# Performance work log

Hardware: AMD Instinct MI355X
Metric: run time of the kernel (lower is better)

## Reference

```python
import jax, jax.numpy as jnp
import numpy as np

NQ = 8  # qubits per circuit (= d_k = n_qubits_ffn)
# Fixed realization of tq.RandomLayer(n_ops=8): 6 parametric rotations + 2 CNOTs
OPS = [("ry", 0), ("rx", 3), ("rz", 5), ("cx", (1, 4)), ("ry", 6), ("rx", 2), ("cx", (0, 7)), ("rz", 4)]
_CNOT = jnp.asarray(np.array([[1,0,0,0],[0,1,0,0],[0,0,0,1],[0,0,1,0]], dtype=np.complex64).reshape(2,2,2,2))
# signs[i, w] = +1 if bit of wire w in basis index i is 0, else -1 (PauliZ eigenvalue)
_idx = np.arange(2 ** NQ)
_bits = (_idx[:, None] >> (NQ - 1 - np.arange(NQ))) & 1
SIGNS = jnp.asarray((1 - 2 * _bits).astype(np.float32))

def _rot(kind, t):
    c = jnp.cos(t / 2).astype(jnp.complex64)
    s = jnp.sin(t / 2).astype(jnp.complex64)
    z = jnp.zeros_like(c)
    if kind == "rx":
        return jnp.stack([jnp.stack([c, -1j * s]), jnp.stack([-1j * s, c])])
    if kind == "ry":
        return jnp.stack([jnp.stack([c, -s]), jnp.stack([s, c])])
    tc = t.astype(jnp.complex64)
    return jnp.stack([jnp.stack([jnp.exp(-1j * tc / 2), z]), jnp.stack([z, jnp.exp(1j * tc / 2)])])

def _apply1(state, U, w):
    st = jnp.tensordot(U, state, axes=((1,), (w + 1,)))
    return jnp.moveaxis(st, 0, w + 1)

def _apply2(state, c, t):  # CNOT, requires c < t (true for OPS)
    st = jnp.tensordot(_CNOT, state, axes=((2, 3), (c + 1, t + 1)))
    return jnp.moveaxis(st, (0, 1), (c + 1, t + 1))

def qcircuit(angles, thetas):
    """angles: [N, NQ] data angles (RX encoding); thetas: [6] gate params.
    Returns PauliZ expectations [N, NQ] (float32)."""
    N = angles.shape[0]
    c = jnp.cos(angles / 2)
    s = jnp.sin(angles / 2)
    amp = jnp.stack([c.astype(jnp.complex64), (-1j) * s.astype(jnp.complex64)], axis=-1)  # [N, NQ, 2]
    # RX-encoded product state |psi> = prod_w RX(x_w)|0>
    state = amp[:, 0]
    for w in range(1, NQ):
        state = state[..., None] * amp[:, w].reshape((N,) + (1,) * w + (2,))
    pi = 0
    for kind, arg in OPS:
        if kind == "cx":
            state = _apply2(state, *arg)
        else:
            state = _apply1(state, _rot(kind, thetas[pi]), arg)
            pi += 1
    probs = jnp.abs(state.reshape(N, -1)) ** 2  # [N, 2^NQ]
    return probs @ SIGNS  # [N, NQ]

def _ln(x, g, b, eps=1e-5):
    m = x.mean(-1, keepdims=True)
    v = ((x - m) ** 2).mean(-1, keepdims=True)
    return (x - m) / jnp.sqrt(v + eps) * g + b

def setup_inputs() -> dict:
    key = jax.random.key(0)
    ks = jax.random.split(key, 8)
    B, S, E, FF = 4, 1024, 64, 256
    return {
        "x": jax.random.normal(ks[0], (B, S, E), dtype=jnp.float32),
        "attn_theta": jax.random.uniform(ks[1], (6,), dtype=jnp.float32, maxval=2 * np.pi),
        "Wc": jax.random.normal(ks[2], (E, E), dtype=jnp.float32) * 0.1,
        "bc": jnp.zeros((E,), jnp.float32),
        "g1": jnp.ones((E,), jnp.float32),
        "beta1": jnp.zeros((E,), jnp.float32),
        "ffn_theta": jax.random.uniform(ks[3], (6,), dtype=jnp.float32, maxval=2 * np.pi),
        "W1": jax.random.normal(ks[4], (NQ, FF), dtype=jnp.float32) * 0.3,
        "b1": jnp.zeros((FF,), jnp.float32),
        "W2": jax.random.normal(ks[5], (FF, E), dtype=jnp.float32) * 0.06,
        "b2": jnp.zeros((E,), jnp.float32),
        "g2": jnp.ones((E,), jnp.float32),
        "beta2": jnp.zeros((E,), jnp.float32),
    }

def reference(x, attn_theta, Wc, bc, g1, beta1, ffn_theta, W1, b1, W2, b2, g2, beta2):
    B, S, E = x.shape
    dk = NQ  # d_k = embed_dim // num_heads = 8
    # --- quantum multi-head attention (same qlayer shared across heads -> vectorize) ---
    q = qcircuit(x.reshape(B * S * (E // dk), dk), attn_theta)  # [B*S*H, dk]
    attn = q.reshape(B, S, E) @ Wc + bc
    y = _ln(x + attn, g1, beta1)
    # --- quantum FFN: encoder uses first NQ features of each token ---
    qf = qcircuit(y.reshape(B * S, E)[:, :NQ], ffn_theta)  # [B*S, NQ]
    h = jax.nn.relu(qf @ W1 + b1)
    ffn = (h @ W2 + b2).reshape(B, S, E)
    return _ln(y + ffn, g2, beta2)
```

## Files before the change

### kernel.cpp

```cpp
#include <hip/hip_runtime.h>


typedef _Float16 h2f   __attribute__((ext_vector_type(2)));
typedef _Float16 f16x8 __attribute__((ext_vector_type(8)));
typedef float    f32x4 __attribute__((ext_vector_type(4)));
typedef int      i32x4 __attribute__((ext_vector_type(4)));

__device__ __forceinline__ int pk(float a, float b) {
    return __builtin_bit_cast(int, __builtin_amdgcn_cvt_pkrtz(a, b));
}
__device__ __forceinline__ float fdot2i(int a, int b, float c) {
    return __builtin_amdgcn_fdot2(__builtin_bit_cast(h2f, a),
                                  __builtin_bit_cast(h2f, b), c, false);
}
__device__ __forceinline__ float rl_f(float v, int l) {
    return __int_as_float(__builtin_amdgcn_readlane(__float_as_int(v), l));
}
__device__ __forceinline__ f16x8 pack8(const float (&v)[8]) {
    i32x4 p;
    p.x = pk(v[0], v[1]);
    p.y = pk(v[2], v[3]);
    p.z = pk(v[4], v[5]);
    p.w = pk(v[6], v[7]);
    return __builtin_bit_cast(f16x8, p);
}
__device__ __forceinline__ void wave_sum2(float& a, float& b) {
#pragma unroll
    for (int m = 32; m > 0; m >>= 1) {
        a += __shfl_xor(a, m, 64);
        b += __shfl_xor(b, m, 64);
    }
}

__global__ __launch_bounds__(512, 2)
void qtb_fused11(const float* __restrict__ x,
                 const float* __restrict__ th_a,
                 const float* __restrict__ Wc,
                 const float* __restrict__ bc,
                 const float* __restrict__ g1,
                 const float* __restrict__ be1,
                 const float* __restrict__ th_f,
                 const float* __restrict__ W1,
                 const float* __restrict__ b1,
                 const float* __restrict__ W2,
                 const float* __restrict__ b2,
                 const float* __restrict__ g2,
                 const float* __restrict__ be2,
                 float* __restrict__ out)
{
    __shared__ __align__(16) int4      sW1[256];
    __shared__ __align__(16) _Float16  sZ[16][72];
    __shared__ __align__(16) float     sA[16][66];
    __shared__ __align__(16) _Float16  sH[16][264];
    __shared__ __align__(16) float     sO[16][66];

    const int tid  = threadIdx.x;
    const int lane = tid & 63;
    const int wv   = tid >> 6;
    const int w    = lane & 7;
    const int gb   = lane & ~7;
    const int tok0 = (blockIdx.x * 8 + wv) * 2;
    const int tl   = wv * 2;
    const int col  = lane & 15;
    const int kg   = lane >> 4;

    float xr[2];
#pragma unroll
    for (int t = 0; t < 2; ++t) xr[t] = x[(tok0 + t) * 64 + lane];

    float bfa[2][8];
    float bff[8][8];
    if (wv < 4) {
        const float* base = Wc + wv * 16 + col;
#pragma unroll
        for (int ks = 0; ks < 2; ++ks)
#pragma unroll
            for (int i = 0; i < 8; ++i)
                bfa[ks][i] = base[(ks * 32 + kg * 8 + i) * 64];
    } else {
        const float* base = W2 + (wv - 4) * 16 + col;
#pragma unroll
        for (int ks = 0; ks < 8; ++ks)
#pragma unroll
            for (int i = 0; i < 8; ++i)
                bff[ks][i] = base[(ks * 32 + kg * 8 + i) * 64];
    }

    if (tid < 64) {
        int j0 = tid * 4;
        float4 r[8];
#pragma unroll
        for (int k = 0; k < 8; ++k) r[k] = *(const float4*)&W1[k * 256 + j0];
        const float* f = (const float*)r;
#pragma unroll
        for (int j = 0; j < 4; ++j)
            sW1[j0 + j] = make_int4(pk(f[0 * 4 + j], f[4 * 4 + j]),
                                    pk(f[1 * 4 + j], f[5 * 4 + j]),
                                    pk(f[2 * 4 + j], f[6 * 4 + j]),
                                    pk(f[3 * 4 + j], f[7 * 4 + j]));
    }

    const float C0a = __cosf(th_a[0]);
    const float T1a = th_a[1];
    const float C3a = __cosf(th_a[3]);
    const float T4a = th_a[4];
    const float C0f = __cosf(th_f[0]);
    const float T1f = th_f[1];
    const float C3f = __cosf(th_f[3]);
    const float T4f = th_f[4];

    const float bcL = bc[lane], g1L = g1[lane], be1L = be1[lane];
    const float b2L = b2[lane], g2L = g2[lane], be2L = be2[lane];
    float b1L[4];
#pragma unroll
    for (int r = 0; r < 4; ++r) b1L[r] = b1[r * 64 + lane];

    const float dA = (w == 2) ? T4a : ((w == 3) ? T1a : 0.0f);
#pragma unroll
    for (int t = 0; t < 2; ++t) {
        float c  = __cosf(xr[t] + dA);
        float c0 = __shfl(c, gb, 64);
        float c1 = __shfl(c, gb + 1, 64);
        float zz = c * ((w == 0) ? C0a : ((w == 6) ? C3a : 1.0f));
        if (w == 4) zz = c * c1;
        if (w == 7) zz = C0a * c0 * c;
        sZ[tl + t][lane] = (_Float16)zz;
    }

    f16x8 bfrag[8];
    if (wv < 4) {
#pragma unroll
        for (int ks = 0; ks < 2; ++ks) bfrag[ks] = pack8(bfa[ks]);
    } else {
#pragma unroll
        for (int ks = 0; ks < 8; ++ks) bfrag[ks] = pack8(bff[ks]);
    }

    __syncthreads();

    if (wv < 4) {
        f32x4 cacc = {0.0f, 0.0f, 0.0f, 0.0f};
#pragma unroll
        for (int ks = 0; ks < 2; ++ks) {
            f16x8 af = *(const f16x8*)&sZ[col][ks * 32 + kg * 8];
            cacc = __builtin_amdgcn_mfma_f32_16x16x32_f16(af, bfrag[ks], cacc, 0, 0, 0);
        }
#pragma unroll
        for (int r = 0; r < 4; ++r)
            sA[kg * 4 + r][wv * 16 + col] = cacc[r];
    }

    __syncthreads();

    float y[2];
#pragma unroll
    for (int t = 0; t < 2; ++t) {
        float v = xr[t] + sA[tl + t][lane] + bcL;
        float s = v, s2 = v * v;
        wave_sum2(s, s2);
        float m   = s * 0.015625f;
        float var = s2 * 0.015625f - m * m;
        y[t] = (v - m) * rsqrtf(var + 1e-5f) * g1L + be1L;
    }

    int4 w1q[4];
#pragma unroll
    for (int r = 0; r < 4; ++r) w1q[r] = sW1[r * 64 + lane];

    const float dF = (w == 2) ? T4f : ((w == 3) ? T1f : 0.0f);
#pragma unroll
    for (int t = 0; t < 2; ++t) {
        float cy = __cosf(y[t] + dF);
        float c0 = rl_f(cy, 0);
        float c1 = rl_f(cy, 1);
        float qz = cy * ((w == 0) ? C0f : ((w == 6) ? C3f : 1.0f));
        if (w == 4) qz = cy * c1;
        if (w == 7) qz = C0f * c0 * cy;
        int qp0 = pk(rl_f(qz, 0), rl_f(qz, 4));
        int qp1 = pk(rl_f(qz, 1), rl_f(qz, 5));
        int qp2 = pk(rl_f(qz, 2), rl_f(qz, 6));
        int qp3 = pk(rl_f(qz, 3), rl_f(qz, 7));
#pragma unroll
        for (int r = 0; r < 4; ++r) {
            float a = b1L[r];
            a = fdot2i(qp0, w1q[r].x, a);
            a = fdot2i(qp1, w1q[r].y, a);
            a = fdot2i(qp2, w1q[r].z, a);
            a = fdot2i(qp3, w1q[r].w, a);
            sH[tl + t][r * 64 + lane] = (_Float16)fmaxf(a, 0.0f);
        }
    }

    __syncthreads();

    if (wv >= 4) {
        f32x4 cacc = {0.0f, 0.0f, 0.0f, 0.0f};
#pragma unroll
        for (int ks = 0; ks < 8; ++ks) {
            f16x8 af = *(const f16x8*)&sH[col][ks * 32 + kg * 8];
            cacc = __builtin_amdgcn_mfma_f32_16x16x32_f16(af, bfrag[ks], cacc, 0, 0, 0);
        }
#pragma unroll
        for (int r = 0; r < 4; ++r)
            sO[kg * 4 + r][(wv - 4) * 16 + col] = cacc[r];
    }

    __syncthreads();

#pragma unroll
    for (int t = 0; t < 2; ++t) {
        float v = y[t] + b2L + sO[tl + t][lane];
        float s = v, s2 = v * v;
        wave_sum2(s, s2);
        float m   = s * 0.015625f;
        float var = s2 * 0.015625f - m * m;
        out[(tok0 + t) * 64 + lane] = (v - m) * rsqrtf(var + 1e-5f) * g2L + be2L;
    }
}

extern "C" void kernel_launch(void* const* d_in, const int* in_sizes, int n_in,
                              void* d_out, int out_size, void* d_ws, size_t ws_size,
                              hipStream_t stream)
{
    const float* x   = (const float*)d_in[0];
    const float* at  = (const float*)d_in[1];
    const float* Wc  = (const float*)d_in[2];
    const float* bcp = (const float*)d_in[3];
    const float* g1  = (const float*)d_in[4];
    const float* be1 = (const float*)d_in[5];
    const float* ft  = (const float*)d_in[6];
    const float* W1  = (const float*)d_in[7];
    const float* b1  = (const float*)d_in[8];
    const float* W2  = (const float*)d_in[9];
    const float* b2  = (const float*)d_in[10];
    const float* g2  = (const float*)d_in[11];
    const float* be2 = (const float*)d_in[12];
    float* out = (float*)d_out;

    qtb_fused11<<<256, 512, 0, stream>>>(x, at, Wc, bcp, g1, be1, ft,
                                         W1, b1, W2, b2, g2, be2, out);
}
```

Before: 9.748 us.

## Halve block size so each wave runs both MFMA stages, and merge LayerNorm reductions

Blocks shrink from 8 waves and 16 tokens to 4 waves and 8 tokens, with twice as many blocks. Every wave now loads both the Wc and W2 fragments and runs both the attention and FFN MFMAs, instead of splitting them across wave groups. The aim is shorter per-block critical paths and more blocks per device. In exchange, half of each 16-row MFMA tile is wasted, and per-wave weight loads and register pressure go up. The two tokens' LayerNorm reductions are also interleaved into a single shuffle loop to add instruction-level parallelism.

```diff
diff --git a/kernel.cpp b/kernel.cpp
--- a/kernel.cpp
+++ b/kernel.cpp
@@ -24,16 +24,18 @@
     p.w = pk(v[6], v[7]);
     return __builtin_bit_cast(f16x8, p);
 }
-__device__ __forceinline__ void wave_sum2(float& a, float& b) {
+__device__ __forceinline__ void wave_sum4(float& a, float& b, float& c, float& d) {
 #pragma unroll
     for (int m = 32; m > 0; m >>= 1) {
         a += __shfl_xor(a, m, 64);
         b += __shfl_xor(b, m, 64);
-    }
-}
-
-__global__ __launch_bounds__(512, 2)
-void qtb_fused11(const float* __restrict__ x,
+        c += __shfl_xor(c, m, 64);
+        d += __shfl_xor(d, m, 64);
+    }
+}
+
+__global__ __launch_bounds__(256, 2)
+void qtb_fused12(const float* __restrict__ x,
                  const float* __restrict__ th_a,
                  const float* __restrict__ Wc,
                  const float* __restrict__ bc,
@@ -59,7 +61,7 @@
     const int wv   = tid >> 6;
     const int w    = lane & 7;
     const int gb   = lane & ~7;
-    const int tok0 = (blockIdx.x * 8 + wv) * 2;
+    const int tok0 = (blockIdx.x * 4 + wv) * 2;
     const int tl   = wv * 2;
     const int col  = lane & 15;
     const int kg   = lane >> 4;
@@ -70,15 +72,16 @@
 
     float bfa[2][8];
     float bff[8][8];
-    if (wv < 4) {
+    {
         const float* base = Wc + wv * 16 + col;
 #pragma unroll
         for (int ks = 0; ks < 2; ++ks)
 #pragma unroll
             for (int i = 0; i < 8; ++i)
                 bfa[ks][i] = base[(ks * 32 + kg * 8 + i) * 64];
-    } else {
-        const float* base = W2 + (wv - 4) * 16 + col;
+    }
+    {
+        const float* base = W2 + wv * 16 + col;
 #pragma unroll
         for (int ks = 0; ks < 8; ++ks)
 #pragma unroll
@@ -127,23 +130,20 @@
         sZ[tl + t][lane] = (_Float16)zz;
     }
 
-    f16x8 bfrag[8];
-    if (wv < 4) {
-#pragma unroll
-        for (int ks = 0; ks < 2; ++ks) bfrag[ks] = pack8(bfa[ks]);
-    } else {
-#pragma unroll
-        for (int ks = 0; ks < 8; ++ks) bfrag[ks] = pack8(bff[ks]);
-    }
-
-    __syncthreads();
-
-    if (wv < 4) {
+    f16x8 bfragA[2], bfragF[8];
+#pragma unroll
+    for (int ks = 0; ks < 2; ++ks) bfragA[ks] = pack8(bfa[ks]);
+#pragma unroll
+    for (int ks = 0; ks < 8; ++ks) bfragF[ks] = pack8(bff[ks]);
+
+    __syncthreads();
+
+    {
         f32x4 cacc = {0.0f, 0.0f, 0.0f, 0.0f};
 #pragma unroll
         for (int ks = 0; ks < 2; ++ks) {
             f16x8 af = *(const f16x8*)&sZ[col][ks * 32 + kg * 8];
-            cacc = __builtin_amdgcn_mfma_f32_16x16x32_f16(af, bfrag[ks], cacc, 0, 0, 0);
+            cacc = __builtin_amdgcn_mfma_f32_16x16x32_f16(af, bfragA[ks], cacc, 0, 0, 0);
         }
 #pragma unroll
         for (int r = 0; r < 4; ++r)
@@ -153,14 +153,16 @@
     __syncthreads();
 
     float y[2];
-#pragma unroll
-    for (int t = 0; t < 2; ++t) {
-        float v = xr[t] + sA[tl + t][lane] + bcL;
-        float s = v, s2 = v * v;
-        wave_sum2(s, s2);
-        float m   = s * 0.015625f;
-        float var = s2 * 0.015625f - m * m;
-        y[t] = (v - m) * rsqrtf(var + 1e-5f) * g1L + be1L;
+    {
+        float v0 = xr[0] + sA[tl + 0][lane] + bcL;
+        float v1 = xr[1] + sA[tl + 1][lane] + bcL;
+        float s0 = v0, q0 = v0 * v0, s1 = v1, q1 = v1 * v1;
+        wave_sum4(s0, q0, s1, q1);
+        float m0 = s0 * 0.015625f, m1 = s1 * 0.015625f;
+        float r0 = rsqrtf(q0 * 0.015625f - m0 * m0 + 1e-5f);
+        float r1 = rsqrtf(q1 * 0.015625f - m1 * m1 + 1e-5f);
+        y[0] = (v0 - m0) * r0 * g1L + be1L;
+        y[1] = (v1 - m1) * r1 * g1L + be1L;
     }
 
     int4 w1q[4];
@@ -193,28 +195,30 @@
 
     __syncthreads();
 
-    if (wv >= 4) {
+    {
         f32x4 cacc = {0.0f, 0.0f, 0.0f, 0.0f};
 #pragma unroll
         for (int ks = 0; ks < 8; ++ks) {
             f16x8 af = *(const f16x8*)&sH[col][ks * 32 + kg * 8];
-            cacc = __builtin_amdgcn_mfma_f32_16x16x32_f16(af, bfrag[ks], cacc, 0, 0, 0);
+            cacc = __builtin_amdgcn_mfma_f32_16x16x32_f16(af, bfragF[ks], cacc, 0, 0, 0);
         }
 #pragma unroll
         for (int r = 0; r < 4; ++r)
-            sO[kg * 4 + r][(wv - 4) * 16 + col] = cacc[r];
-    }
-
-    __syncthreads();
-
-#pragma unroll
-    for (int t = 0; t < 2; ++t) {
-        float v = y[t] + b2L + sO[tl + t][lane];
-        float s = v, s2 = v * v;
-        wave_sum2(s, s2);
-        float m   = s * 0.015625f;
-        float var = s2 * 0.015625f - m * m;
-        out[(tok0 + t) * 64 + lane] = (v - m) * rsqrtf(var + 1e-5f) * g2L + be2L;
+            sO[kg * 4 + r][wv * 16 + col] = cacc[r];
+    }
+
+    __syncthreads();
+
+    {
+        float v0 = y[0] + b2L + sO[tl + 0][lane];
+        float v1 = y[1] + b2L + sO[tl + 1][lane];
+        float s0 = v0, q0 = v0 * v0, s1 = v1, q1 = v1 * v1;
+        wave_sum4(s0, q0, s1, q1);
+        float m0 = s0 * 0.015625f, m1 = s1 * 0.015625f;
+        float r0 = rsqrtf(q0 * 0.015625f - m0 * m0 + 1e-5f);
+        float r1 = rsqrtf(q1 * 0.015625f - m1 * m1 + 1e-5f);
+        out[(tok0 + 0) * 64 + lane] = (v0 - m0) * r0 * g2L + be2L;
+        out[(tok0 + 1) * 64 + lane] = (v1 - m1) * r1 * g2L + be2L;
     }
 }
 
@@ -237,6 +241,6 @@
     const float* be2 = (const float*)d_in[12];
     float* out = (float*)d_out;
 
-    qtb_fused11<<<256, 512, 0, stream>>>(x, at, Wc, bcp, g1, be1, ft,
+    qtb_fused12<<<512, 256, 0, stream>>>(x, at, Wc, bcp, g1, be1, ft,
                                          W1, b1, W2, b2, g2, be2, out);
 }
```

Result: slower. 10.38 us (+6.5%).
